# Performance work log

Measured on AMD Instinct MI355X. Metric: run time of the kernel, lower is better.

Reference implementation:

```python
import jax, jax.numpy as jnp
import numpy as np

NEG_INF = 1e9  # matches module's -1000000000.0 masking constant


def setup_inputs() -> dict:
    key = jax.random.key(0)
    kq, kv = jax.random.split(key)
    B, T, D = 4, 2048, 1024
    query = jax.random.normal(kq, (B, T, D), dtype=jnp.float32)
    value = jax.random.normal(kv, (B, T, D), dtype=jnp.float32)
    return {"query": query, "value": value}


def reference(query, value):
    # key defaults to value (len(inputs) == 2 path)
    k = value
    # dot-product scores (canonical Keras Attention _calculate_scores)
    scores = jnp.einsum("bqd,bkd->bqk", query, k)  # [B, Tq, Tv]
    Tq, Tv = scores.shape[-2], scores.shape[-1]
    # causal lower-triangular mask over last two dims (row >= col)
    causal_mask = jnp.tril(jnp.ones((Tq, Tv), dtype=bool))  # [Tq, Tv]
    # scores -= 1e9 * (~mask), then softmax (eval mode: no dropout)
    scores = scores - NEG_INF * (~causal_mask).astype(scores.dtype)
    weights = jax.nn.softmax(scores, axis=-1)
    result = jnp.einsum("bqv,bvd->bqd", weights, value)
    return result
```

## Files before the change

kernel.cpp:

```cpp
#include <hip/hip_runtime.h>
#include <hip/hip_fp16.h>

typedef _Float16 half8 __attribute__((ext_vector_type(8)));
typedef _Float16 half4v __attribute__((ext_vector_type(4)));
typedef float    floatx4 __attribute__((ext_vector_type(4)));

#define MFMA16(a, b, c) __builtin_amdgcn_mfma_f32_16x16x32_f16((a), (b), (c), 0, 0, 0)

constexpr int T_ = 2048;
constexpr int D_ = 1024;
constexpr int NB = 4;
constexpr int NTILE = 136;
constexpr size_t TILE_ELEMS = 16384;

__device__ __forceinline__ half8 cvt8(floatx4 a, floatx4 b) {
  half8 h;
  h[0] = (_Float16)a[0]; h[1] = (_Float16)a[1]; h[2] = (_Float16)a[2]; h[3] = (_Float16)a[3];
  h[4] = (_Float16)b[0]; h[5] = (_Float16)b[1]; h[6] = (_Float16)b[2]; h[7] = (_Float16)b[3];
  return h;
}

__device__ __forceinline__ void gl16(const void* g, void* l) {
  __builtin_amdgcn_global_load_lds(
      (const __attribute__((address_space(1))) void*)g,
      (__attribute__((address_space(3))) void*)l, 16, 0, 0);
}

__device__ __forceinline__ void STEP_SYNC() {
  asm volatile("s_waitcnt vmcnt(0)" ::: "memory");
  __builtin_amdgcn_s_barrier();
  __builtin_amdgcn_sched_barrier(0);
}

__global__ __launch_bounds__(256) void cast_q(const float* __restrict__ Q,
                                              _Float16* __restrict__ Qh) {
  const size_t i = ((size_t)blockIdx.x * 256 + threadIdx.x) * 8;
  *(half8*)(Qh + i) = cvt8(*(const floatx4*)(Q + i), *(const floatx4*)(Q + i + 4));
}

__global__ __launch_bounds__(256) void build_vt(const float* __restrict__ V,
                                                _Float16* __restrict__ VhT) {
  __shared__ _Float16 tile[64][65];
  const int bid = blockIdx.x;
  const int b = bid & 3, tt = (bid >> 2) & 31, dd = bid >> 7;
  const float* Vb = V + ((size_t)b * T_ + tt * 64) * D_ + dd * 64;
#pragma unroll
  for (int k = 0; k < 16; ++k) {
    const int e = k * 256 + threadIdx.x, r = e >> 6, c = e & 63;
    tile[r][c] = (_Float16)Vb[(size_t)r * D_ + c];
  }
  __syncthreads();
#pragma unroll
  for (int k = 0; k < 16; ++k) {
    const int e = k * 256 + threadIdx.x, dr = e >> 6, tc = e & 63;
    VhT[((size_t)b * D_ + dd * 64 + dr) * T_ + tt * 64 + tc] = tile[tc][dr];
  }
}

__global__ __launch_bounds__(256, 3) void sgemm(const _Float16* __restrict__ Qh,
                                                const float* __restrict__ V,
                                                float* __restrict__ Sp) {
  __shared__ __align__(16) char lds[49152];
  const int tid = threadIdx.x;
  const int w = tid >> 6, l = tid & 63, l15 = l & 15, hi = l >> 4;
  const int wr = (w >> 1) * 64, wc = (w & 1) * 64;
  const int l2 = l >> 2, l3 = l >> 3;

  const int b = (int)(blockIdx.x & 3);
  int rem = (int)(blockIdx.x >> 2), j = 0;
  while (rem >= 16 - j) { rem -= 16 - j; ++j; }
  const int i = j + rem;

  const _Float16* Qb = Qh + ((size_t)(b * T_ + i * 128)) * D_;
  const float*    Vb = V  + ((size_t)(b * T_ + j * 128)) * D_;

  auto STAGE = [&](const int s, const int buf) {
    char* Ad = lds + buf * 24576 + w * 2048;
    char* Bd = lds + buf * 24576 + 8192 + w * 4096;
#pragma unroll
    for (int q = 0; q < 2; ++q) {
      const int ar = w * 32 + q * 16 + l2;
      const int sw = (ar + (ar >> 2)) & 3;
      gl16(Qb + (size_t)ar * D_ + s * 32 + (((l & 3) ^ sw) << 3), Ad + q * 1024);
    }
#pragma unroll
    for (int q = 0; q < 4; ++q) {
      const int br = w * 32 + q * 8 + l3;
      gl16(Vb + (size_t)br * D_ + s * 32 + (((l & 7) ^ (br & 7)) << 2), Bd + q * 1024);
    }
  };

  floatx4 acc[4][4];
#pragma unroll
  for (int mi = 0; mi < 4; ++mi)
#pragma unroll
    for (int ni = 0; ni < 4; ++ni) acc[mi][ni] = (floatx4){0.f, 0.f, 0.f, 0.f};

  STAGE(0, 0);
  STEP_SYNC();
  for (int s = 0; s < 32; ++s) {
    const int buf = s & 1;
    if (s + 1 < 32) STAGE(s + 1, buf ^ 1);
    const char* Ab = lds + buf * 24576;
    const char* Bb = lds + buf * 24576 + 8192;
    half8 af[4], bb[4];
#pragma unroll
    for (int mi = 0; mi < 4; ++mi) {
      const int row = wr + mi * 16 + l15;
      const int sw = (row + (row >> 2)) & 3;
      af[mi] = *(const half8*)(Ab + row * 64 + ((hi ^ sw) << 4));
    }
#pragma unroll
    for (int ni = 0; ni < 4; ++ni) {
      const int row = wc + ni * 16 + l15;
      const int p0 = (hi << 1) ^ (row & 7);
      const floatx4 f0 = *(const floatx4*)(Bb + row * 128 + (p0 << 4));
      const floatx4 f1 = *(const floatx4*)(Bb + row * 128 + ((p0 ^ 1) << 4));
      bb[ni] = cvt8(f0, f1);
    }
#pragma unroll
    for (int mi = 0; mi < 4; ++mi)
#pragma unroll
      for (int ni = 0; ni < 4; ++ni)
        acc[mi][ni] = MFMA16(af[mi], bb[ni], acc[mi][ni]);
    STEP_SYNC();
  }

  float* tp = Sp + (size_t)(b * NTILE + ((i * (i + 1)) >> 1) + j) * TILE_ELEMS;
#pragma unroll
  for (int mi = 0; mi < 4; ++mi)
#pragma unroll
    for (int r = 0; r < 4; ++r) {
      const int row = wr + mi * 16 + 4 * hi + r;
#pragma unroll
      for (int ni = 0; ni < 4; ++ni)
        tp[row * 128 + wc + ni * 16 + l15] = acc[mi][ni][r];
    }
}

__global__ __launch_bounds__(256) void smax(float* __restrict__ Sp,
                                            float* __restrict__ lrow) {
  const int b = (int)(blockIdx.x & 3), t = (int)(blockIdx.x >> 2);
  const int wv = threadIdx.x >> 6, l = threadIdx.x & 63;
  const int l32 = l & 31;
  const int row = 2040 - t * 8 + wv * 2 + (l >> 5);
  const int i = row >> 7, r = row & 127;
  char* tb0 = (char*)(Sp + (size_t)(b * NTILE + ((i * (i + 1)) >> 1)) * TILE_ELEMS);

  float mx = -1e30f;
  for (int j = 0; j <= i; ++j) {
    const floatx4 v = *(const floatx4*)(tb0 + (size_t)j * 65536 + r * 512 + l32 * 16);
    const int col0 = j * 128 + l32 * 4;
#pragma unroll
    for (int e = 0; e < 4; ++e)
      if (col0 + e <= row) mx = fmaxf(mx, v[e]);
  }
#pragma unroll
  for (int off = 1; off < 32; off <<= 1) mx = fmaxf(mx, __shfl_xor(mx, off));

  float sum = 0.f;
  for (int j = 0; j <= i; ++j) {
    char* tbj = tb0 + (size_t)j * 65536;
    const floatx4 v = *(const floatx4*)(tbj + r * 512 + l32 * 16);
    const int col0 = j * 128 + l32 * 4;
    half4v hv;
#pragma unroll
    for (int e = 0; e < 4; ++e) {
      const float p = (col0 + e <= row) ? __expf(v[e] - mx) : 0.f;
      sum += p;
      hv[e] = (_Float16)p;
    }
    *(half4v*)(tbj + r * 512 + l32 * 8) = hv;
  }
#pragma unroll
  for (int off = 1; off < 32; off <<= 1) sum += __shfl_xor(sum, off);
  if (l32 == 0) lrow[b * 2048 + row] = sum;
}

__global__ __launch_bounds__(256, 3) void pv(const float* __restrict__ Sp,
                                             const _Float16* __restrict__ VhT,
                                             const float* __restrict__ lrow,
                                             float* __restrict__ O) {
  __shared__ __align__(16) char lds[32768];
  __shared__ float Lsh[128];
  const int tid = threadIdx.x;
  const int w = tid >> 6, l = tid & 63, l15 = l & 15, hi = l >> 4;
  const int wr = (w >> 1) * 64, wc = (w & 1) * 64;
  const int l2 = l >> 2;

  const int b = (int)(blockIdx.x & 3), t = (int)(blockIdx.x >> 2);
  const int r_ = t >> 3;
  const int i = (r_ < 8) ? (15 - r_) : (r_ - 8);
  const int nc = t & 7;
  const int ns = (i + 1) * 4;

  const char* Pbase = (const char*)(Sp + (size_t)(b * NTILE + ((i * (i + 1)) >> 1)) * TILE_ELEMS);
  const _Float16* Vt = VhT + ((size_t)(b * D_ + nc * 128)) * T_;
  if (tid < 128) Lsh[tid] = lrow[b * 2048 + i * 128 + tid];

  auto STAGE = [&](const int s, const int buf) {
    char* Ad = lds + buf * 16384 + w * 2048;
    char* Bd = lds + buf * 16384 + 8192 + w * 2048;
#pragma unroll
    for (int q = 0; q < 2; ++q) {
      const int ar = w * 32 + q * 16 + l2;
      const int sw = (ar + (ar >> 2)) & 3;
      gl16(Pbase + (size_t)(s >> 2) * 65536 + ar * 512 + (s & 3) * 64 +
               (((l & 3) ^ sw) << 4),
           Ad + q * 1024);
      gl16(Vt + (size_t)ar * T_ + s * 32 + (((l & 3) ^ sw) << 3), Bd + q * 1024);
    }
  };

  floatx4 acc[4][4];
#pragma unroll
  for (int mi = 0; mi < 4; ++mi)
#pragma unroll
    for (int ni = 0; ni < 4; ++ni) acc[mi][ni] = (floatx4){0.f, 0.f, 0.f, 0.f};

  STAGE(0, 0);
  STEP_SYNC();
  for (int s = 0; s < ns; ++s) {
    const int buf = s & 1;
    if (s + 1 < ns) STAGE(s + 1, buf ^ 1);
    const char* Ab = lds + buf * 16384;
    const char* Bb = lds + buf * 16384 + 8192;
    half8 af[4], bb[4];
#pragma unroll
    for (int mi = 0; mi < 4; ++mi) {
      const int row = wr + mi * 16 + l15;
      const int sw = (row + (row >> 2)) & 3;
      af[mi] = *(const half8*)(Ab + row * 64 + ((hi ^ sw) << 4));
    }
#pragma unroll
    for (int ni = 0; ni < 4; ++ni) {
      const int row = wc + ni * 16 + l15;
      const int sw = (row + (row >> 2)) & 3;
      bb[ni] = *(const half8*)(Bb + row * 64 + ((hi ^ sw) << 4));
    }
#pragma unroll
    for (int mi = 0; mi < 4; ++mi)
#pragma unroll
      for (int ni = 0; ni < 4; ++ni)
        acc[mi][ni] = MFMA16(af[mi], bb[ni], acc[mi][ni]);
    STEP_SYNC();
  }

  float* Ob = O + ((size_t)b * T_ + i * 128) * D_ + nc * 128;
#pragma unroll
  for (int mi = 0; mi < 4; ++mi)
#pragma unroll
    for (int r = 0; r < 4; ++r) {
      const int rl = wr + mi * 16 + 4 * hi + r;
      const float inv = 1.0f / Lsh[rl];
#pragma unroll
      for (int ni = 0; ni < 4; ++ni)
        Ob[(size_t)rl * D_ + wc + ni * 16 + l15] = acc[mi][ni][r] * inv;
    }
}

__global__ __launch_bounds__(256) void attn_fb(const float* __restrict__ Q,
                                               const float* __restrict__ V,
                                               float* __restrict__ O) {
  __shared__ float sc[2048];
  __shared__ float red[4];
  const int b = (int)(blockIdx.x >> 11), m = (int)(blockIdx.x & 2047);
  const int tid = threadIdx.x;
  const float* Qr = Q + ((size_t)b * T_ + m) * D_;
  for (int kv = tid; kv <= m; kv += 256) {
    const float* Vr = V + ((size_t)b * T_ + kv) * D_;
    float s = 0.f;
    for (int d = 0; d < D_; d += 4) {
      floatx4 q4 = *(const floatx4*)(Qr + d), v4 = *(const floatx4*)(Vr + d);
      s += q4[0] * v4[0] + q4[1] * v4[1] + q4[2] * v4[2] + q4[3] * v4[3];
    }
    sc[kv] = s;
  }
  __syncthreads();
  float mx = -1e30f;
  for (int kv = tid; kv <= m; kv += 256) mx = fmaxf(mx, sc[kv]);
#pragma unroll
  for (int off = 1; off < 64; off <<= 1) mx = fmaxf(mx, __shfl_xor(mx, off));
  if ((tid & 63) == 0) red[tid >> 6] = mx;
  __syncthreads();
  mx = fmaxf(fmaxf(red[0], red[1]), fmaxf(red[2], red[3]));
  __syncthreads();
  float sum = 0.f;
  for (int kv = tid; kv <= m; kv += 256) { float p = __expf(sc[kv] - mx); sc[kv] = p; sum += p; }
#pragma unroll
  for (int off = 1; off < 64; off <<= 1) sum += __shfl_xor(sum, off);
  __syncthreads();
  if ((tid & 63) == 0) red[tid >> 6] = sum;
  __syncthreads();
  const float inv = 1.0f / (red[0] + red[1] + red[2] + red[3]);
  float* Or = O + ((size_t)b * T_ + m) * D_;
  const int d = tid * 4;
  floatx4 o = {0.f, 0.f, 0.f, 0.f};
  for (int kv = 0; kv <= m; ++kv) {
    const float p = sc[kv];
    const floatx4 v4 = *(const floatx4*)(V + ((size_t)b * T_ + kv) * D_ + d);
    o[0] += p * v4[0]; o[1] += p * v4[1]; o[2] += p * v4[2]; o[3] += p * v4[3];
  }
  o[0] *= inv; o[1] *= inv; o[2] *= inv; o[3] *= inv;
  *(floatx4*)(Or + d) = o;
}

extern "C" void kernel_launch(void* const* d_in, const int* in_sizes, int n_in,
                              void* d_out, int out_size, void* d_ws, size_t ws_size,
                              hipStream_t stream) {
  const float* q = (const float*)d_in[0];
  const float* v = (const float*)d_in[1];
  float* out = (float*)d_out;

  const size_t OFF_S = 16777216;
  const size_t OFF_L = OFF_S + (size_t)NB * NTILE * TILE_ELEMS * 4;
  const size_t NEED = OFF_L + (size_t)NB * 2048 * 4;

  if (ws_size >= NEED) {
    _Float16* fh = (_Float16*)d_ws;
    float* Sp = (float*)((char*)d_ws + OFF_S);
    float* lr = (float*)((char*)d_ws + OFF_L);
    cast_q<<<dim3(4096), dim3(256), 0, stream>>>(q, fh);
    sgemm<<<dim3(NB * NTILE), dim3(256), 0, stream>>>(fh, v, Sp);
    smax<<<dim3(1024), dim3(256), 0, stream>>>(Sp, lr);
    build_vt<<<dim3(2048), dim3(256), 0, stream>>>(v, fh);
    pv<<<dim3(512), dim3(256), 0, stream>>>(Sp, fh, lr, out);
  } else {
    attn_fb<<<dim3(NB * T_), dim3(256), 0, stream>>>(q, v, out);
  }
}
```

Baseline: 113.8 us.

## Triple-buffer LDS staging with partial vmcnt waits in sgemm and pv

Converts the double-buffered global-to-LDS pipelines in the QK^T and PV GEMMs into three-stage rotating buffers with prefetch distance two. Each iteration now waits only for the oldest stage's loads (vmcnt(6) or vmcnt(4)) and uses a single barrier per step instead of two full-drain syncs. This is meant to hide more global-load latency behind the MFMA work. In exchange LDS use grows, and sgemm's occupancy hint drops from 3 to 2 blocks per CU.

```diff
diff --git a/kernel.cpp b/kernel.cpp
--- a/kernel.cpp
+++ b/kernel.cpp
@@ -24,12 +24,6 @@
   __builtin_amdgcn_global_load_lds(
       (const __attribute__((address_space(1))) void*)g,
       (__attribute__((address_space(3))) void*)l, 16, 0, 0);
-}
-
-__device__ __forceinline__ void STEP_SYNC() {
-  asm volatile("s_waitcnt vmcnt(0)" ::: "memory");
-  __builtin_amdgcn_s_barrier();
-  __builtin_amdgcn_sched_barrier(0);
 }
 
 __global__ __launch_bounds__(256) void cast_q(const float* __restrict__ Q,
@@ -57,10 +51,10 @@
   }
 }
 
-__global__ __launch_bounds__(256, 3) void sgemm(const _Float16* __restrict__ Qh,
+__global__ __launch_bounds__(256, 2) void sgemm(const _Float16* __restrict__ Qh,
                                                 const float* __restrict__ V,
                                                 float* __restrict__ Sp) {
-  __shared__ __align__(16) char lds[49152];
+  __shared__ __align__(16) char lds[73728];
   const int tid = threadIdx.x;
   const int w = tid >> 6, l = tid & 63, l15 = l & 15, hi = l >> 4;
   const int wr = (w >> 1) * 64, wc = (w & 1) * 64;
@@ -97,12 +91,16 @@
     for (int ni = 0; ni < 4; ++ni) acc[mi][ni] = (floatx4){0.f, 0.f, 0.f, 0.f};
 
   STAGE(0, 0);
-  STEP_SYNC();
+  STAGE(1, 1);
+  int bc = 0, bp = 2;
   for (int s = 0; s < 32; ++s) {
-    const int buf = s & 1;
-    if (s + 1 < 32) STAGE(s + 1, buf ^ 1);
-    const char* Ab = lds + buf * 24576;
-    const char* Bb = lds + buf * 24576 + 8192;
+    if (s < 31) { asm volatile("s_waitcnt vmcnt(6)" ::: "memory"); }
+    else        { asm volatile("s_waitcnt vmcnt(0)" ::: "memory"); }
+    __builtin_amdgcn_s_barrier();
+    __builtin_amdgcn_sched_barrier(0);
+    if (s + 2 < 32) STAGE(s + 2, bp);
+    const char* Ab = lds + bc * 24576;
+    const char* Bb = lds + bc * 24576 + 8192;
     half8 af[4], bb[4];
 #pragma unroll
     for (int mi = 0; mi < 4; ++mi) {
@@ -123,7 +121,8 @@
 #pragma unroll
       for (int ni = 0; ni < 4; ++ni)
         acc[mi][ni] = MFMA16(af[mi], bb[ni], acc[mi][ni]);
-    STEP_SYNC();
+    bc = (bc == 2) ? 0 : bc + 1;
+    bp = (bp == 2) ? 0 : bp + 1;
   }
 
   float* tp = Sp + (size_t)(b * NTILE + ((i * (i + 1)) >> 1) + j) * TILE_ELEMS;
@@ -181,7 +180,7 @@
                                              const _Float16* __restrict__ VhT,
                                              const float* __restrict__ lrow,
                                              float* __restrict__ O) {
-  __shared__ __align__(16) char lds[32768];
+  __shared__ __align__(16) char lds[49152];
   __shared__ float Lsh[128];
   const int tid = threadIdx.x;
   const int w = tid >> 6, l = tid & 63, l15 = l & 15, hi = l >> 4;
@@ -219,12 +218,16 @@
     for (int ni = 0; ni < 4; ++ni) acc[mi][ni] = (floatx4){0.f, 0.f, 0.f, 0.f};
 
   STAGE(0, 0);
-  STEP_SYNC();
+  STAGE(1, 1);
+  int bc = 0, bp = 2;
   for (int s = 0; s < ns; ++s) {
-    const int buf = s & 1;
-    if (s + 1 < ns) STAGE(s + 1, buf ^ 1);
-    const char* Ab = lds + buf * 16384;
-    const char* Bb = lds + buf * 16384 + 8192;
+    if (s < ns - 1) { asm volatile("s_waitcnt vmcnt(4)" ::: "memory"); }
+    else            { asm volatile("s_waitcnt vmcnt(0)" ::: "memory"); }
+    __builtin_amdgcn_s_barrier();
+    __builtin_amdgcn_sched_barrier(0);
+    if (s + 2 < ns) STAGE(s + 2, bp);
+    const char* Ab = lds + bc * 16384;
+    const char* Bb = lds + bc * 16384 + 8192;
     half8 af[4], bb[4];
 #pragma unroll
     for (int mi = 0; mi < 4; ++mi) {
@@ -243,7 +246,8 @@
 #pragma unroll
       for (int ni = 0; ni < 4; ++ni)
         acc[mi][ni] = MFMA16(af[mi], bb[ni], acc[mi][ni]);
-    STEP_SYNC();
+    bc = (bc == 2) ? 0 : bc + 1;
+    bp = (bp == 2) ? 0 : bp + 1;
   }
 
   float* Ob = O + ((size_t)b * T_ + i * 128) * D_ + nc * 128;
```

Result: slower. 122.1 us (+7.3%).

## Halve GEMM tiles, drop LDS double-buffering to raise block count and occupancy

Applied to the files above, without the earlier changes.

Both the QK^T score GEMM and the PV GEMM now use smaller per-block tiles: 64x128 for sgemm (272 tiles per batch) and 128x64 for pv (1024 blocks). The double-buffered LDS pipeline with explicit vmcnt waits is replaced by a single buffer with __syncthreads. Launch bounds rise to 4 blocks per SM. The aim is more blocks in flight and better load balance on the triangular workload. In exchange, operand reuse per block drops and the prefetch overlap between loads and MFMA is lost.

```diff
diff --git a/kernel.cpp b/kernel.cpp
--- a/kernel.cpp
+++ b/kernel.cpp
@@ -24,12 +24,6 @@
   __builtin_amdgcn_global_load_lds(
       (const __attribute__((address_space(1))) void*)g,
       (__attribute__((address_space(3))) void*)l, 16, 0, 0);
-}
-
-__device__ __forceinline__ void STEP_SYNC() {
-  asm volatile("s_waitcnt vmcnt(0)" ::: "memory");
-  __builtin_amdgcn_s_barrier();
-  __builtin_amdgcn_sched_barrier(0);
 }
 
 __global__ __launch_bounds__(256) void cast_q(const float* __restrict__ Q,
@@ -57,78 +51,70 @@
   }
 }
 
-__global__ __launch_bounds__(256, 3) void sgemm(const _Float16* __restrict__ Qh,
+__global__ __launch_bounds__(256, 4) void sgemm(const _Float16* __restrict__ Qh,
                                                 const float* __restrict__ V,
                                                 float* __restrict__ Sp) {
-  __shared__ __align__(16) char lds[49152];
+  __shared__ __align__(16) char As[4096];
+  __shared__ __align__(16) char Bs[16384];
   const int tid = threadIdx.x;
   const int w = tid >> 6, l = tid & 63, l15 = l & 15, hi = l >> 4;
-  const int wr = (w >> 1) * 64, wc = (w & 1) * 64;
-  const int l2 = l >> 2, l3 = l >> 3;
+  const int wr = (w >> 1) * 32, wc = (w & 1) * 64;
 
   const int b = (int)(blockIdx.x & 3);
   int rem = (int)(blockIdx.x >> 2), j = 0;
-  while (rem >= 16 - j) { rem -= 16 - j; ++j; }
-  const int i = j + rem;
-
-  const _Float16* Qb = Qh + ((size_t)(b * T_ + i * 128)) * D_;
+  while (rem >= 32 - 2 * j) { rem -= 32 - 2 * j; ++j; }
+  const int i64 = 2 * j + rem;
+  const int I = i64 >> 1;
+
+  const _Float16* Qb = Qh + ((size_t)(b * T_ + i64 * 64)) * D_;
   const float*    Vb = V  + ((size_t)(b * T_ + j * 128)) * D_;
 
-  auto STAGE = [&](const int s, const int buf) {
-    char* Ad = lds + buf * 24576 + w * 2048;
-    char* Bd = lds + buf * 24576 + 8192 + w * 4096;
-#pragma unroll
-    for (int q = 0; q < 2; ++q) {
-      const int ar = w * 32 + q * 16 + l2;
-      const int sw = (ar + (ar >> 2)) & 3;
-      gl16(Qb + (size_t)ar * D_ + s * 32 + (((l & 3) ^ sw) << 3), Ad + q * 1024);
-    }
-#pragma unroll
-    for (int q = 0; q < 4; ++q) {
-      const int br = w * 32 + q * 8 + l3;
-      gl16(Vb + (size_t)br * D_ + s * 32 + (((l & 7) ^ (br & 7)) << 2), Bd + q * 1024);
-    }
-  };
-
-  floatx4 acc[4][4];
-#pragma unroll
-  for (int mi = 0; mi < 4; ++mi)
+  const int arow = w * 16 + (l >> 2);
+  const int aoff = ((((arow + (arow >> 2)) & 3) ^ (l & 3)) << 3);
+  const int brow0 = w * 32 + (l >> 3);
+  const int boff = (((l & 7) ^ (l >> 3)) << 2);
+  char* Adst = As + w * 1024;
+  char* Bdst = Bs + w * 4096;
+
+  floatx4 acc[2][4];
+#pragma unroll
+  for (int mi = 0; mi < 2; ++mi)
 #pragma unroll
     for (int ni = 0; ni < 4; ++ni) acc[mi][ni] = (floatx4){0.f, 0.f, 0.f, 0.f};
 
-  STAGE(0, 0);
-  STEP_SYNC();
   for (int s = 0; s < 32; ++s) {
-    const int buf = s & 1;
-    if (s + 1 < 32) STAGE(s + 1, buf ^ 1);
-    const char* Ab = lds + buf * 24576;
-    const char* Bb = lds + buf * 24576 + 8192;
-    half8 af[4], bb[4];
-#pragma unroll
-    for (int mi = 0; mi < 4; ++mi) {
+    gl16(Qb + (size_t)arow * D_ + s * 32 + aoff, Adst);
+#pragma unroll
+    for (int q = 0; q < 4; ++q)
+      gl16(Vb + (size_t)(brow0 + q * 8) * D_ + s * 32 + boff, Bdst + q * 1024);
+    __syncthreads();
+    half8 af[2], bb[4];
+#pragma unroll
+    for (int mi = 0; mi < 2; ++mi) {
       const int row = wr + mi * 16 + l15;
       const int sw = (row + (row >> 2)) & 3;
-      af[mi] = *(const half8*)(Ab + row * 64 + ((hi ^ sw) << 4));
+      af[mi] = *(const half8*)(As + row * 64 + ((hi ^ sw) << 4));
     }
 #pragma unroll
     for (int ni = 0; ni < 4; ++ni) {
       const int row = wc + ni * 16 + l15;
       const int p0 = (hi << 1) ^ (row & 7);
-      const floatx4 f0 = *(const floatx4*)(Bb + row * 128 + (p0 << 4));
-      const floatx4 f1 = *(const floatx4*)(Bb + row * 128 + ((p0 ^ 1) << 4));
+      const floatx4 f0 = *(const floatx4*)(Bs + row * 128 + (p0 << 4));
+      const floatx4 f1 = *(const floatx4*)(Bs + row * 128 + ((p0 ^ 1) << 4));
       bb[ni] = cvt8(f0, f1);
     }
 #pragma unroll
-    for (int mi = 0; mi < 4; ++mi)
+    for (int mi = 0; mi < 2; ++mi)
 #pragma unroll
       for (int ni = 0; ni < 4; ++ni)
         acc[mi][ni] = MFMA16(af[mi], bb[ni], acc[mi][ni]);
-    STEP_SYNC();
-  }
-
-  float* tp = Sp + (size_t)(b * NTILE + ((i * (i + 1)) >> 1) + j) * TILE_ELEMS;
-#pragma unroll
-  for (int mi = 0; mi < 4; ++mi)
+    __syncthreads();
+  }
+
+  float* tp = Sp + (size_t)(b * NTILE + ((I * (I + 1)) >> 1) + j) * TILE_ELEMS +
+              (i64 & 1) * 8192;
+#pragma unroll
+  for (int mi = 0; mi < 2; ++mi)
 #pragma unroll
     for (int r = 0; r < 4; ++r) {
       const int row = wr + mi * 16 + 4 * hi + r;
@@ -177,85 +163,80 @@
   if (l32 == 0) lrow[b * 2048 + row] = sum;
 }
 
-__global__ __launch_bounds__(256, 3) void pv(const float* __restrict__ Sp,
+__global__ __launch_bounds__(256, 4) void pv(const float* __restrict__ Sp,
                                              const _Float16* __restrict__ VhT,
                                              const float* __restrict__ lrow,
                                              float* __restrict__ O) {
-  __shared__ __align__(16) char lds[32768];
+  __shared__ __align__(16) char As[8192];
+  __shared__ __align__(16) char Bs[4096];
   __shared__ float Lsh[128];
   const int tid = threadIdx.x;
   const int w = tid >> 6, l = tid & 63, l15 = l & 15, hi = l >> 4;
-  const int wr = (w >> 1) * 64, wc = (w & 1) * 64;
-  const int l2 = l >> 2;
-
-  const int b = (int)(blockIdx.x & 3), t = (int)(blockIdx.x >> 2);
-  const int r_ = t >> 3;
-  const int i = (r_ < 8) ? (15 - r_) : (r_ - 8);
-  const int nc = t & 7;
+  const int wr = w * 32;
+
+  const int b = (int)(blockIdx.x & 3);
+  const int u = (int)(blockIdx.x >> 2);
+  const int iidx = (u + (u >> 4)) & 15;
+  const int i = (iidx < 8) ? (15 - iidx) : (iidx - 8);
+  const int nc = u >> 4;
   const int ns = (i + 1) * 4;
 
   const char* Pbase = (const char*)(Sp + (size_t)(b * NTILE + ((i * (i + 1)) >> 1)) * TILE_ELEMS);
-  const _Float16* Vt = VhT + ((size_t)(b * D_ + nc * 128)) * T_;
+  const _Float16* Vt = VhT + ((size_t)(b * D_ + nc * 64)) * T_;
   if (tid < 128) Lsh[tid] = lrow[b * 2048 + i * 128 + tid];
 
-  auto STAGE = [&](const int s, const int buf) {
-    char* Ad = lds + buf * 16384 + w * 2048;
-    char* Bd = lds + buf * 16384 + 8192 + w * 2048;
+  const int vrow = w * 16 + (l >> 2);
+  const int voff = ((((vrow + (vrow >> 2)) & 3) ^ (l & 3)) << 3);
+  char* Adst = As + w * 2048;
+  char* Bdst = Bs + w * 1024;
+
+  floatx4 acc[2][4];
+#pragma unroll
+  for (int mi = 0; mi < 2; ++mi)
+#pragma unroll
+    for (int ni = 0; ni < 4; ++ni) acc[mi][ni] = (floatx4){0.f, 0.f, 0.f, 0.f};
+
+  for (int s = 0; s < ns; ++s) {
 #pragma unroll
     for (int q = 0; q < 2; ++q) {
-      const int ar = w * 32 + q * 16 + l2;
-      const int sw = (ar + (ar >> 2)) & 3;
-      gl16(Pbase + (size_t)(s >> 2) * 65536 + ar * 512 + (s & 3) * 64 +
-               (((l & 3) ^ sw) << 4),
-           Ad + q * 1024);
-      gl16(Vt + (size_t)ar * T_ + s * 32 + (((l & 3) ^ sw) << 3), Bd + q * 1024);
-    }
-  };
-
-  floatx4 acc[4][4];
-#pragma unroll
-  for (int mi = 0; mi < 4; ++mi)
-#pragma unroll
-    for (int ni = 0; ni < 4; ++ni) acc[mi][ni] = (floatx4){0.f, 0.f, 0.f, 0.f};
-
-  STAGE(0, 0);
-  STEP_SYNC();
-  for (int s = 0; s < ns; ++s) {
-    const int buf = s & 1;
-    if (s + 1 < ns) STAGE(s + 1, buf ^ 1);
-    const char* Ab = lds + buf * 16384;
-    const char* Bb = lds + buf * 16384 + 8192;
-    half8 af[4], bb[4];
-#pragma unroll
-    for (int mi = 0; mi < 4; ++mi) {
+      const int ar = w * 32 + q * 16 + (l >> 2);
+      const int sw = (((ar + (ar >> 2)) & 3) ^ (l & 3)) << 4;
+      gl16(Pbase + (size_t)(s >> 2) * 65536 + ar * 512 + (s & 3) * 64 + sw,
+           Adst + q * 1024);
+    }
+    gl16(Vt + (size_t)vrow * T_ + s * 32 + voff, Bdst);
+    __syncthreads();
+    half8 af[2], bb[4];
+#pragma unroll
+    for (int mi = 0; mi < 2; ++mi) {
       const int row = wr + mi * 16 + l15;
       const int sw = (row + (row >> 2)) & 3;
-      af[mi] = *(const half8*)(Ab + row * 64 + ((hi ^ sw) << 4));
+      af[mi] = *(const half8*)(As + row * 64 + ((hi ^ sw) << 4));
     }
 #pragma unroll
     for (int ni = 0; ni < 4; ++ni) {
-      const int row = wc + ni * 16 + l15;
+      const int row = ni * 16 + l15;
       const int sw = (row + (row >> 2)) & 3;
-      bb[ni] = *(const half8*)(Bb + row * 64 + ((hi ^ sw) << 4));
-    }
-#pragma unroll
-    for (int mi = 0; mi < 4; ++mi)
+      bb[ni] = *(const half8*)(Bs + row * 64 + ((hi ^ sw) << 4));
+    }
+#pragma unroll
+    for (int mi = 0; mi < 2; ++mi)
 #pragma unroll
       for (int ni = 0; ni < 4; ++ni)
         acc[mi][ni] = MFMA16(af[mi], bb[ni], acc[mi][ni]);
-    STEP_SYNC();
-  }
-
-  float* Ob = O + ((size_t)b * T_ + i * 128) * D_ + nc * 128;
-#pragma unroll
-  for (int mi = 0; mi < 4; ++mi)
+    __syncthreads();
+  }
+
+  float* Ob = O + ((size_t)b * T_ + i * 128) * D_ + nc * 64;
+#pragma unroll
+  for (int mi = 0; mi < 2; ++mi)
 #pragma unroll
     for (int r = 0; r < 4; ++r) {
       const int rl = wr + mi * 16 + 4 * hi + r;
       const float inv = 1.0f / Lsh[rl];
 #pragma unroll
       for (int ni = 0; ni < 4; ++ni)
-        Ob[(size_t)rl * D_ + wc + ni * 16 + l15] = acc[mi][ni][r] * inv;
+        Ob[(size_t)rl * D_ + ni * 16 + l15] = acc[mi][ni][r] * inv;
     }
 }
 
@@ -321,10 +302,10 @@
     float* Sp = (float*)((char*)d_ws + OFF_S);
     float* lr = (float*)((char*)d_ws + OFF_L);
     cast_q<<<dim3(4096), dim3(256), 0, stream>>>(q, fh);
-    sgemm<<<dim3(NB * NTILE), dim3(256), 0, stream>>>(fh, v, Sp);
+    sgemm<<<dim3(NB * 272), dim3(256), 0, stream>>>(fh, v, Sp);
     smax<<<dim3(1024), dim3(256), 0, stream>>>(Sp, lr);
     build_vt<<<dim3(2048), dim3(256), 0, stream>>>(v, fh);
-    pv<<<dim3(512), dim3(256), 0, stream>>>(Sp, fh, lr, out);
+    pv<<<dim3(1024), dim3(256), 0, stream>>>(Sp, fh, lr, out);
   } else {
     attn_fb<<<dim3(NB * T_), dim3(256), 0, stream>>>(q, v, out);
   }
```

Result: slower. 122.0 us (+7.2%).
